# Performance work log

Hardware: AMD Instinct MI355X
Metric: run time of the kernel (lower is better)

Reference implementation:

```python
import jax, jax.numpy as jnp
import numpy as np

EMBED = 256; HEADS = 8; LEVELS = 4; POINTS = 4; DIM = EMBED // HEADS


def _bilinear_gather(vflat, H, W, px, py):
    """grid_sample(mode='bilinear', padding='zeros', align_corners=False).
    vflat: (bs, heads, H*W, d); px, py: (bs, heads, nq, P) pixel coords.
    Returns (bs, heads, nq, P, d).
    """
    x0 = jnp.floor(px); y0 = jnp.floor(py)
    x1 = x0 + 1.0;      y1 = y0 + 1.0
    wx1 = px - x0; wx0 = 1.0 - wx1
    wy1 = py - y0; wy0 = 1.0 - wy1

    def corner(ix, iy, w):
        valid = (ix >= 0) & (ix <= W - 1) & (iy >= 0) & (iy <= H - 1)
        idx = (jnp.clip(iy, 0, H - 1) * W + jnp.clip(ix, 0, W - 1)).astype(jnp.int32)
        b, h, nq, P = idx.shape
        g = jnp.take_along_axis(vflat, idx.reshape(b, h, nq * P)[..., None], axis=2)
        g = g.reshape(b, h, nq, P, -1)
        return g * (w * valid)[..., None]

    return (corner(x0, y0, wx0 * wy0) + corner(x1, y0, wx1 * wy0)
            + corner(x0, y1, wx0 * wy1) + corner(x1, y1, wx1 * wy1))


def _ms_deform_attn(value4, shapes, loc, attn):
    """value4 (bs,nv,heads,D); loc (bs,nq,heads,L,P,2) in [0,1];
    attn (bs,nq,heads,L,P). Returns (bs,nq,heads*D)."""
    bs, nq = loc.shape[0], loc.shape[1]
    grids = 2.0 * loc - 1.0
    attn_t = jnp.transpose(attn, (0, 2, 1, 3, 4))  # (bs,heads,nq,L,P)
    out = jnp.zeros((bs, HEADS, nq, DIM), value4.dtype)
    start = 0
    for lvl in range(LEVELS):
        H, W = int(shapes[lvl, 0]), int(shapes[lvl, 1])
        v = value4[:, start:start + H * W]                 # (bs,HW,heads,D)
        vflat = jnp.transpose(v, (0, 2, 1, 3))             # (bs,heads,HW,D)
        g = jnp.transpose(grids[:, :, :, lvl], (0, 2, 1, 3, 4))  # (bs,heads,nq,P,2)
        px = (g[..., 0] + 1.0) * (W * 0.5) - 0.5
        py = (g[..., 1] + 1.0) * (H * 0.5) - 0.5
        sampled = _bilinear_gather(vflat, H, W, px, py)    # (bs,heads,nq,P,D)
        out = out + jnp.einsum('bhqpd,bhqp->bhqd', sampled, attn_t[:, :, :, lvl])
        start += H * W
    return jnp.transpose(out, (0, 2, 1, 3)).reshape(bs, nq, HEADS * DIM)


def _forward(query, value, query_pos, reference_points, last_reference_offsets,
             shapes, Wv, bv, Wo, bo, Wa, ba, Wout, bout):
    identity = query
    q = query + query_pos
    bs, nq, _ = q.shape
    nv = value.shape[1]
    v = (value @ Wv + bv).reshape(bs, nv, HEADS, DIM)
    off = (q @ Wo + bo).reshape(bs, nq, HEADS, LEVELS, POINTS, 2)
    attn = jax.nn.softmax((q @ Wa + ba).reshape(bs, nq, HEADS, LEVELS * POINTS), axis=-1)
    attn = attn.reshape(bs, nq, HEADS, LEVELS, POINTS)
    wh = jnp.asarray(np.asarray(shapes)[:, ::-1].copy(), jnp.float32)  # (L,2) as (w,h)
    loc = (reference_points[:, :, None, :, None, :]
           + off / wh[None, None, None, :, None, :]
           + last_reference_offsets[:, :, :, None, None, :])  # flow-guided per-head shift
    out = _ms_deform_attn(v, shapes, loc, attn)
    return out @ Wout + bout + identity  # dropout is identity at eval


def setup_inputs() -> dict:
    key = jax.random.key(0)
    ks = jax.random.split(key, 10)
    bs, nq = 8, 1200
    shapes = np.array([[92, 160], [46, 80], [23, 40], [12, 20]], np.int64)
    nv = int((shapes[:, 0] * shapes[:, 1]).sum())
    f = jnp.float32
    return {
        "query": jax.random.normal(ks[0], (bs, nq, EMBED), f),
        "value": jax.random.normal(ks[1], (bs, nv, EMBED), f),
        "query_pos": jax.random.normal(ks[2], (bs, nq, EMBED), f),
        "reference_points": jax.random.uniform(ks[3], (bs, nq, LEVELS, 2), f),
        "last_reference_offsets": jax.random.normal(ks[4], (bs, nq, HEADS, 2), f) * 0.02,
        "spatial_shapes": shapes,
        "Wv": jax.random.normal(ks[5], (EMBED, EMBED), f) * 0.02,
        "bv": jnp.zeros((EMBED,), f),
        "Wo": jax.random.normal(ks[6], (EMBED, HEADS * LEVELS * POINTS * 2), f) * 0.02,
        "bo": jax.random.normal(ks[7], (HEADS * LEVELS * POINTS * 2,), f) * 0.02,
        "Wa": jax.random.normal(ks[8], (EMBED, HEADS * LEVELS * POINTS), f) * 0.02,
        "ba": jnp.zeros((HEADS * LEVELS * POINTS,), f),
        "Wout": jax.random.normal(ks[9], (EMBED, EMBED), f) * 0.02,
        "bout": jnp.zeros((EMBED,), f),
    }


def reference(query, value, query_pos, reference_points, last_reference_offsets,
              spatial_shapes, Wv, bv, Wo, bo, Wa, ba, Wout, bout):
    return _forward(query, value, query_pos, reference_points, last_reference_offsets,
                    spatial_shapes, Wv, bv, Wo, bo, Wa, ba, Wout, bout)
```

## Files before the change

kernel.cpp:

```cpp
#include <hip/hip_runtime.h>
#include <math.h>

#define BS 8
#define NQ 1200
#define NV 19560
#define EMB 256

typedef __bf16 bf16;
typedef bf16 bf16x8 __attribute__((ext_vector_type(8)));
typedef float f32x4 __attribute__((ext_vector_type(4)));
typedef float f32x16 __attribute__((ext_vector_type(16)));

static __device__ __forceinline__ bf16x8 cvt8(float4 a, float4 b) {
    bf16x8 r;
    r[0] = (bf16)a.x; r[1] = (bf16)a.y; r[2] = (bf16)a.z; r[3] = (bf16)a.w;
    r[4] = (bf16)b.x; r[5] = (bf16)b.y; r[6] = (bf16)b.z; r[7] = (bf16)b.w;
    return r;
}

static __device__ __forceinline__ void gl16(const void* g, void* l) {
    __builtin_amdgcn_global_load_lds(
        (const __attribute__((address_space(1))) void*)g,
        (__attribute__((address_space(3))) void*)l, 16, 0, 0);
}

__global__ __launch_bounds__(256) void prep_k(
    const float* __restrict__ Wv, const float* __restrict__ Wo,
    const float* __restrict__ Wa, const float* __restrict__ Wout,
    const float* __restrict__ query, const float* __restrict__ qpos,
    bf16* __restrict__ Wv_p, bf16* __restrict__ Wo_p,
    bf16* __restrict__ Wa_p, bf16* __restrict__ Wout_p, bf16* __restrict__ qsum)
{
    int bid = blockIdx.x, tid = threadIdx.x;
    if (bid < 896) {
        const float* src; bf16* dst; int N, t0;
        if (bid < 256)      { src = Wv;   dst = Wv_p;   N = 256; t0 = bid * 256; }
        else if (bid < 512) { src = Wo;   dst = Wo_p;   N = 256; t0 = (bid - 256) * 256; }
        else if (bid < 640) { src = Wa;   dst = Wa_p;   N = 128; t0 = (bid - 512) * 256; }
        else                { src = Wout; dst = Wout_p; N = 256; t0 = (bid - 640) * 256; }
        int t = t0 + tid;
        int n = t >> 8, k = t & 255;
        dst[t] = (bf16)src[k * N + n];
    } else {
        int t = (bid - 896) * 256 + tid;
        qsum[t] = (bf16)(query[t] + qpos[t]);
    }
}

__global__ __launch_bounds__(256, 1) void vgemm_k(
    const float* __restrict__ A, const bf16* __restrict__ Bp,
    const float* __restrict__ bias, bf16* __restrict__ outB, int Mtiles)
{
    __shared__ __align__(16) bf16 sB[256 * 256];
    const int tid = threadIdx.x;
    const int lane = tid & 63;
    const int w = tid >> 6;
    const int l32 = lane & 31;
    const int hi = lane >> 5;
    const int wr = w >> 1, wc = w & 1;
    const int tstride = gridDim.x;

    float4 buf0[32], buf1[32];
    auto loadA = [&](int t, float4* d) {
        const float* src = A + ((size_t)t * 64 + wr * 32 + l32) * 256 + hi * 8;
#pragma unroll
        for (int ks = 0; ks < 16; ++ks) {
            d[2 * ks]     = *(const float4*)(src + ks * 16);
            d[2 * ks + 1] = *(const float4*)(src + ks * 16 + 4);
        }
    };

    int t0 = blockIdx.x;
    loadA(t0, buf0);

#pragma unroll
    for (int i = 0; i < 32; ++i) {
        int s = i * 256 + tid;
        int r = s >> 5, p = s & 31, c = p ^ (r & 7);
        gl16(Bp + (size_t)r * 256 + c * 8, sB + ((size_t)i * 256 + w * 64) * 8);
    }

    float bb[4];
#pragma unroll
    for (int ct = 0; ct < 4; ++ct) bb[ct] = bias[wc * 128 + ct * 32 + l32];

    __syncthreads();

    auto comp = [&](int t, const float4* d) {
        f32x16 acc[4];
#pragma unroll
        for (int ct = 0; ct < 4; ++ct)
#pragma unroll
            for (int rg = 0; rg < 16; ++rg) acc[ct][rg] = 0.f;
#pragma unroll
        for (int ks = 0; ks < 16; ++ks) {
            bf16x8 af = cvt8(d[2 * ks], d[2 * ks + 1]);
            int p = (ks * 2 + hi) ^ (l32 & 7);
#pragma unroll
            for (int ct = 0; ct < 4; ++ct) {
                int r = wc * 128 + ct * 32 + l32;
                bf16x8 bfr = *(const bf16x8*)(sB + (size_t)r * 256 + p * 8);
                acc[ct] = __builtin_amdgcn_mfma_f32_32x32x16_bf16(af, bfr, acc[ct], 0, 0, 0);
            }
        }
#pragma unroll
        for (int ct = 0; ct < 4; ++ct) {
            int col = wc * 128 + ct * 32 + l32;
#pragma unroll
            for (int rg = 0; rg < 16; ++rg) {
                int row = t * 64 + wr * 32 + (rg & 3) + 8 * (rg >> 2) + 4 * hi;
                outB[(size_t)row * 256 + col] = (bf16)(acc[ct][rg] + bb[ct]);
            }
        }
    };

    int t = t0;
    while (t < Mtiles) {
        int t1 = t + tstride;
        if (t1 < Mtiles) loadA(t1, buf1);
        comp(t, buf0);
        if (t1 >= Mtiles) break;
        int t2 = t1 + tstride;
        if (t2 < Mtiles) loadA(t2, buf0);
        comp(t1, buf1);
        if (t2 >= Mtiles) break;
        t = t2;
    }
}

template <int NS, int NB, bool HAS_RES, bool OUT_BF16>
__global__ __launch_bounds__(256, 2) void gemm3_k(
    const bf16* __restrict__ Ah, const bf16* __restrict__ Bp,
    const float* __restrict__ bias, const float* __restrict__ res,
    float* __restrict__ outF, bf16* __restrict__ outB, int Mtiles)
{
    constexpr int CT = NB / 16;
    __shared__ __align__(16) bf16 sB[NB * 256];
    const int tid = threadIdx.x;
    const int lane = tid & 63;
    const int w = tid >> 6;
    const int l16 = lane & 15;
    const int qd = lane >> 4;
    const int col0 = (blockIdx.x & 1) * NB;
    const int tstride = gridDim.x >> 1;
    const bf16* Bsrc = Bp + (size_t)col0 * 256;

    uint4 curH[8], nxtH[8];
    auto loadA = [&](int t, uint4* dH) {
        size_t rb = ((size_t)t * 64 + w * 16 + l16) * 256;
#pragma unroll
        for (int kc = 0; kc < 8; ++kc)
            dH[kc] = *(const uint4*)(Ah + rb + kc * 32 + qd * 8);
    };

    int tile = blockIdx.x >> 1;
    if (tile < Mtiles) loadA(tile, curH);

#pragma unroll
    for (int i = 0; i < NB * 32 / 256; ++i) {
        int s = i * 256 + tid;
        int r = s >> 5, p = s & 31, c = p ^ (r & 7);
        gl16(Bsrc + (size_t)r * 256 + c * 8, sB + (size_t)(i * 256 + w * 64) * 8);
    }
    __syncthreads();

    for (; tile < Mtiles; tile += tstride) {
        int nt = tile + tstride;
        if (nt < Mtiles) loadA(nt, nxtH);

        f32x4 acc[CT];
#pragma unroll
        for (int c = 0; c < CT; ++c) acc[c] = (f32x4){0.f, 0.f, 0.f, 0.f};
#pragma unroll
        for (int kc = 0; kc < 8; ++kc) {
            bf16x8 af = *(const bf16x8*)&curH[kc];
#pragma unroll
            for (int ct = 0; ct < CT; ++ct) {
                int brow = ct * 16 + l16;
                int chunk = (kc * 4 + qd) ^ (l16 & 7);
                bf16x8 bfr = *(const bf16x8*)(sB + (size_t)brow * 256 + chunk * 8);
                acc[ct] = __builtin_amdgcn_mfma_f32_16x16x32_bf16(af, bfr, acc[ct], 0, 0, 0);
            }
        }
#pragma unroll
        for (int ct = 0; ct < CT; ++ct) {
            int col = col0 + ct * 16 + l16;
            float bbv = bias[col];
#pragma unroll
            for (int r = 0; r < 4; ++r) {
                int row = tile * 64 + w * 16 + qd * 4 + r;
                size_t idx = (size_t)row * NS + col;
                float v = acc[ct][r] + bbv;
                if (HAS_RES) v += res[idx];
                if (OUT_BF16) outB[idx] = (bf16)v;
                else          outF[idx] = v;
            }
        }
#pragma unroll
        for (int i = 0; i < 8; ++i) curH[i] = nxtH[i];
    }
}

static __device__ __forceinline__ void b8f(uint4 u, float* f) {
    f[0] = __uint_as_float(u.x << 16); f[1] = __uint_as_float(u.x & 0xffff0000u);
    f[2] = __uint_as_float(u.y << 16); f[3] = __uint_as_float(u.y & 0xffff0000u);
    f[4] = __uint_as_float(u.z << 16); f[5] = __uint_as_float(u.z & 0xffff0000u);
    f[6] = __uint_as_float(u.w << 16); f[7] = __uint_as_float(u.w & 0xffff0000u);
}

__global__ __launch_bounds__(256) void sample3_k(
    const bf16* __restrict__ vv, const float* __restrict__ offb,
    const float* __restrict__ attnb, const float* __restrict__ refp,
    const float* __restrict__ lref, bf16* __restrict__ outb)
{
    const int cH[4] = {92, 46, 23, 12};
    const int cW[4] = {160, 80, 40, 20};
    const int cS[4] = {0, 14720, 18400, 19320};
    int tid = threadIdx.x;
    int ql = tid >> 5;
    int l32 = tid & 31;
    int h = l32 >> 2, dg = l32 & 3;
    int bq = blockIdx.x * 8 + ql;
    int b = bq / NQ;

    const float* ap = attnb + (size_t)bq * 128 + h * 16;
    float wgt[16];
    float mx = -1e30f;
#pragma unroll
    for (int i = 0; i < 16; i++) { wgt[i] = ap[i]; mx = fmaxf(mx, wgt[i]); }
    float s = 0.f;
#pragma unroll
    for (int i = 0; i < 16; i++) { wgt[i] = __expf(wgt[i] - mx); s += wgt[i]; }
    float inv = 1.f / s;

    const float* rp = refp + (size_t)bq * 8;
    float lrx = lref[(size_t)bq * 16 + h * 2 + 0];
    float lry = lref[(size_t)bq * 16 + h * 2 + 1];
    const float* op = offb + (size_t)bq * 256 + h * 32;

    float acc[8] = {0.f, 0.f, 0.f, 0.f, 0.f, 0.f, 0.f, 0.f};
#pragma unroll
    for (int lvl = 0; lvl < 4; ++lvl) {
        const int Hh = cH[lvl], Ww = cW[lvl];
        const bf16* vb = vv + ((size_t)b * NV + cS[lvl]) * 256 + h * 32 + dg * 8;
        float rx = rp[lvl * 2 + 0], ry = rp[lvl * 2 + 1];
#pragma unroll
        for (int p = 0; p < 4; ++p) {
            float ox = op[lvl * 8 + p * 2 + 0];
            float oy = op[lvl * 8 + p * 2 + 1];
            float px = (rx + ox / (float)Ww + lrx) * (float)Ww - 0.5f;
            float py = (ry + oy / (float)Hh + lry) * (float)Hh - 0.5f;
            float x0f = floorf(px), y0f = floorf(py);
            int x0 = (int)x0f, y0 = (int)y0f;
            float wx1 = px - x0f, wx0 = 1.f - wx1;
            float wy1 = py - y0f, wy0 = 1.f - wy1;
            float ww = wgt[lvl * 4 + p] * inv;
            float w00 = ww * wx0 * wy0, w01 = ww * wx1 * wy0;
            float w10 = ww * wx0 * wy1, w11 = ww * wx1 * wy1;
            bool xa = (unsigned)x0 < (unsigned)Ww;
            bool xb = (unsigned)(x0 + 1) < (unsigned)Ww;
            bool ya = (unsigned)y0 < (unsigned)Hh;
            bool yb = (unsigned)(y0 + 1) < (unsigned)Hh;
            float f[8];
            if (xa && ya) {
                b8f(*(const uint4*)(vb + ((size_t)y0 * Ww + x0) * 256), f);
#pragma unroll
                for (int j = 0; j < 8; j++) acc[j] = fmaf(w00, f[j], acc[j]);
            }
            if (xb && ya) {
                b8f(*(const uint4*)(vb + ((size_t)y0 * Ww + x0 + 1) * 256), f);
#pragma unroll
                for (int j = 0; j < 8; j++) acc[j] = fmaf(w01, f[j], acc[j]);
            }
            if (xa && yb) {
                b8f(*(const uint4*)(vb + ((size_t)(y0 + 1) * Ww + x0) * 256), f);
#pragma unroll
                for (int j = 0; j < 8; j++) acc[j] = fmaf(w10, f[j], acc[j]);
            }
            if (xb && yb) {
                b8f(*(const uint4*)(vb + ((size_t)(y0 + 1) * Ww + x0 + 1) * 256), f);
#pragma unroll
                for (int j = 0; j < 8; j++) acc[j] = fmaf(w11, f[j], acc[j]);
            }
        }
    }
    bf16x8 o;
#pragma unroll
    for (int j = 0; j < 8; j++) o[j] = (bf16)acc[j];
    *(bf16x8*)(outb + (size_t)bq * 256 + h * 32 + dg * 8) = o;
}

extern "C" void kernel_launch(void* const* d_in, const int* in_sizes, int n_in,
                              void* d_out, int out_size, void* d_ws, size_t ws_size,
                              hipStream_t stream) {
    (void)in_sizes; (void)n_in; (void)out_size; (void)ws_size;
    const float* query = (const float*)d_in[0];
    const float* value = (const float*)d_in[1];
    const float* qpos  = (const float*)d_in[2];
    const float* refp  = (const float*)d_in[3];
    const float* lref  = (const float*)d_in[4];
    const float* Wv   = (const float*)d_in[6];
    const float* bv   = (const float*)d_in[7];
    const float* Wo   = (const float*)d_in[8];
    const float* bo   = (const float*)d_in[9];
    const float* Wa   = (const float*)d_in[10];
    const float* ba   = (const float*)d_in[11];
    const float* Wout = (const float*)d_in[12];
    const float* bout = (const float*)d_in[13];

    char* ws = (char*)d_ws;
    bf16*  Wv_p   = (bf16*)(ws + 0);
    bf16*  Wo_p   = (bf16*)(ws + 131072);
    bf16*  Wa_p   = (bf16*)(ws + 262144);
    bf16*  Wout_p = (bf16*)(ws + 327680);
    bf16*  qsum   = (bf16*)(ws + 458752);
    float* off_b  = (float*)(ws + 5373952);
    float* attn_b = (float*)(ws + 15204352);
    bf16*  tsa_b  = (bf16*)(ws + 20119552);
    bf16*  v_b    = (bf16*)(ws + 25034752);

    prep_k<<<10496, 256, 0, stream>>>(Wv, Wo, Wa, Wout, query, qpos,
                                      Wv_p, Wo_p, Wa_p, Wout_p, qsum);

    vgemm_k<<<256, 256, 0, stream>>>(value, Wv_p, bv, v_b, (BS * NV) / 64);
    gemm3_k<256, 128, false, false><<<300, 256, 0, stream>>>(
        qsum, Wo_p, bo, nullptr, off_b, nullptr, (BS * NQ) / 64);
    gemm3_k<128, 64, false, false><<<300, 256, 0, stream>>>(
        qsum, Wa_p, ba, nullptr, attn_b, nullptr, (BS * NQ) / 64);
    sample3_k<<<(BS * NQ) / 8, 256, 0, stream>>>(v_b, off_b, attn_b, refp, lref, tsa_b);
    gemm3_k<256, 128, true, false><<<300, 256, 0, stream>>>(
        tsa_b, Wout_p, bout, query, (float*)d_out, nullptr, (BS * NQ) / 64);
}
```

Before: 416.7 us.

## Parallelize deformable sampling across sampling points with wave-level shuffle reductions

The sampling kernel now gives each 64-lane wave one (query, head) pair, with lanes split over the 16 level/point samples and 4 channel groups, where before one thread looped serially over all 16 samples. Softmax and the final accumulation are done with cross-lane xor shuffles. Corner loads are issued unconditionally at clamped indices, with validity masks folded into the weights, so the four gathers are branch-free and can all be in flight at once. This raises memory-level parallelism and occupancy for the gather-bound kernel. The cost is extra shuffle reductions, 16x more threads, and loads for out-of-bounds corners that were previously skipped.

```diff
diff --git a/kernel.cpp b/kernel.cpp
--- a/kernel.cpp
+++ b/kernel.cpp
@@ -208,7 +208,7 @@
     f[6] = __uint_as_float(u.w << 16); f[7] = __uint_as_float(u.w & 0xffff0000u);
 }
 
-__global__ __launch_bounds__(256) void sample3_k(
+__global__ __launch_bounds__(256) void sample4_k(
     const bf16* __restrict__ vv, const float* __restrict__ offb,
     const float* __restrict__ attnb, const float* __restrict__ refp,
     const float* __restrict__ lref, bf16* __restrict__ outb)
@@ -216,78 +216,78 @@
     const int cH[4] = {92, 46, 23, 12};
     const int cW[4] = {160, 80, 40, 20};
     const int cS[4] = {0, 14720, 18400, 19320};
-    int tid = threadIdx.x;
-    int ql = tid >> 5;
-    int l32 = tid & 31;
-    int h = l32 >> 2, dg = l32 & 3;
-    int bq = blockIdx.x * 8 + ql;
-    int b = bq / NQ;
-
-    const float* ap = attnb + (size_t)bq * 128 + h * 16;
-    float wgt[16];
-    float mx = -1e30f;
-#pragma unroll
-    for (int i = 0; i < 16; i++) { wgt[i] = ap[i]; mx = fmaxf(mx, wgt[i]); }
-    float s = 0.f;
-#pragma unroll
-    for (int i = 0; i < 16; i++) { wgt[i] = __expf(wgt[i] - mx); s += wgt[i]; }
-    float inv = 1.f / s;
-
-    const float* rp = refp + (size_t)bq * 8;
-    float lrx = lref[(size_t)bq * 16 + h * 2 + 0];
+    const int w = threadIdx.x >> 6;
+    const int lane = threadIdx.x & 63;
+    const int wid = blockIdx.x * 4 + w;
+    const int bq = wid >> 3, h = wid & 7;
+    const int b = bq / NQ;
+    const int p = lane >> 2, dg = lane & 3;
+    const int lvl = p >> 2;
+
+    float logit = attnb[(size_t)bq * 128 + h * 16 + p];
+    float mx = logit;
+#pragma unroll
+    for (int s = 4; s < 64; s <<= 1) mx = fmaxf(mx, __shfl_xor(mx, s));
+    float e = __expf(logit - mx);
+    float ssum = e;
+#pragma unroll
+    for (int s = 4; s < 64; s <<= 1) ssum += __shfl_xor(ssum, s);
+    float wgt = e / ssum;
+
+    const int Hh = cH[lvl], Ww = cW[lvl];
+    float ox = offb[(size_t)bq * 256 + h * 32 + p * 2];
+    float oy = offb[(size_t)bq * 256 + h * 32 + p * 2 + 1];
+    float rx = refp[(size_t)bq * 8 + lvl * 2];
+    float ry = refp[(size_t)bq * 8 + lvl * 2 + 1];
+    float lrx = lref[(size_t)bq * 16 + h * 2];
     float lry = lref[(size_t)bq * 16 + h * 2 + 1];
-    const float* op = offb + (size_t)bq * 256 + h * 32;
-
-    float acc[8] = {0.f, 0.f, 0.f, 0.f, 0.f, 0.f, 0.f, 0.f};
-#pragma unroll
-    for (int lvl = 0; lvl < 4; ++lvl) {
-        const int Hh = cH[lvl], Ww = cW[lvl];
-        const bf16* vb = vv + ((size_t)b * NV + cS[lvl]) * 256 + h * 32 + dg * 8;
-        float rx = rp[lvl * 2 + 0], ry = rp[lvl * 2 + 1];
-#pragma unroll
-        for (int p = 0; p < 4; ++p) {
-            float ox = op[lvl * 8 + p * 2 + 0];
-            float oy = op[lvl * 8 + p * 2 + 1];
-            float px = (rx + ox / (float)Ww + lrx) * (float)Ww - 0.5f;
-            float py = (ry + oy / (float)Hh + lry) * (float)Hh - 0.5f;
-            float x0f = floorf(px), y0f = floorf(py);
-            int x0 = (int)x0f, y0 = (int)y0f;
-            float wx1 = px - x0f, wx0 = 1.f - wx1;
-            float wy1 = py - y0f, wy0 = 1.f - wy1;
-            float ww = wgt[lvl * 4 + p] * inv;
-            float w00 = ww * wx0 * wy0, w01 = ww * wx1 * wy0;
-            float w10 = ww * wx0 * wy1, w11 = ww * wx1 * wy1;
-            bool xa = (unsigned)x0 < (unsigned)Ww;
-            bool xb = (unsigned)(x0 + 1) < (unsigned)Ww;
-            bool ya = (unsigned)y0 < (unsigned)Hh;
-            bool yb = (unsigned)(y0 + 1) < (unsigned)Hh;
-            float f[8];
-            if (xa && ya) {
-                b8f(*(const uint4*)(vb + ((size_t)y0 * Ww + x0) * 256), f);
-#pragma unroll
-                for (int j = 0; j < 8; j++) acc[j] = fmaf(w00, f[j], acc[j]);
-            }
-            if (xb && ya) {
-                b8f(*(const uint4*)(vb + ((size_t)y0 * Ww + x0 + 1) * 256), f);
-#pragma unroll
-                for (int j = 0; j < 8; j++) acc[j] = fmaf(w01, f[j], acc[j]);
-            }
-            if (xa && yb) {
-                b8f(*(const uint4*)(vb + ((size_t)(y0 + 1) * Ww + x0) * 256), f);
-#pragma unroll
-                for (int j = 0; j < 8; j++) acc[j] = fmaf(w10, f[j], acc[j]);
-            }
-            if (xb && yb) {
-                b8f(*(const uint4*)(vb + ((size_t)(y0 + 1) * Ww + x0 + 1) * 256), f);
-#pragma unroll
-                for (int j = 0; j < 8; j++) acc[j] = fmaf(w11, f[j], acc[j]);
-            }
-        }
-    }
-    bf16x8 o;
-#pragma unroll
-    for (int j = 0; j < 8; j++) o[j] = (bf16)acc[j];
-    *(bf16x8*)(outb + (size_t)bq * 256 + h * 32 + dg * 8) = o;
+
+    float px = (rx + ox / (float)Ww + lrx) * (float)Ww - 0.5f;
+    float py = (ry + oy / (float)Hh + lry) * (float)Hh - 0.5f;
+    float x0f = floorf(px), y0f = floorf(py);
+    int x0 = (int)x0f, y0 = (int)y0f;
+    float wx1 = px - x0f, wx0 = 1.f - wx1;
+    float wy1 = py - y0f, wy0 = 1.f - wy1;
+    bool xa = (unsigned)x0 < (unsigned)Ww, xb = (unsigned)(x0 + 1) < (unsigned)Ww;
+    bool ya = (unsigned)y0 < (unsigned)Hh, yb = (unsigned)(y0 + 1) < (unsigned)Hh;
+    int xc0 = min(max(x0, 0), Ww - 1), xc1 = min(max(x0 + 1, 0), Ww - 1);
+    int yc0 = min(max(y0, 0), Hh - 1), yc1 = min(max(y0 + 1, 0), Hh - 1);
+    float w00 = wgt * wx0 * wy0 * (float)(xa && ya);
+    float w01 = wgt * wx1 * wy0 * (float)(xb && ya);
+    float w10 = wgt * wx0 * wy1 * (float)(xa && yb);
+    float w11 = wgt * wx1 * wy1 * (float)(xb && yb);
+
+    const bf16* vb = vv + ((size_t)b * NV + cS[lvl]) * 256 + h * 32 + dg * 8;
+    uint4 g00 = *(const uint4*)(vb + ((size_t)yc0 * Ww + xc0) * 256);
+    uint4 g01 = *(const uint4*)(vb + ((size_t)yc0 * Ww + xc1) * 256);
+    uint4 g10 = *(const uint4*)(vb + ((size_t)yc1 * Ww + xc0) * 256);
+    uint4 g11 = *(const uint4*)(vb + ((size_t)yc1 * Ww + xc1) * 256);
+
+    float acc[8], f[8];
+    b8f(g00, f);
+#pragma unroll
+    for (int j = 0; j < 8; j++) acc[j] = w00 * f[j];
+    b8f(g01, f);
+#pragma unroll
+    for (int j = 0; j < 8; j++) acc[j] = fmaf(w01, f[j], acc[j]);
+    b8f(g10, f);
+#pragma unroll
+    for (int j = 0; j < 8; j++) acc[j] = fmaf(w10, f[j], acc[j]);
+    b8f(g11, f);
+#pragma unroll
+    for (int j = 0; j < 8; j++) acc[j] = fmaf(w11, f[j], acc[j]);
+
+#pragma unroll
+    for (int s = 4; s < 64; s <<= 1)
+#pragma unroll
+        for (int j = 0; j < 8; j++) acc[j] += __shfl_xor(acc[j], s);
+
+    if (p == 0) {
+        bf16x8 o;
+#pragma unroll
+        for (int j = 0; j < 8; j++) o[j] = (bf16)acc[j];
+        *(bf16x8*)(outb + (size_t)bq * 256 + h * 32 + dg * 8) = o;
+    }
 }
 
 extern "C" void kernel_launch(void* const* d_in, const int* in_sizes, int n_in,
@@ -327,7 +327,7 @@
         qsum, Wo_p, bo, nullptr, off_b, nullptr, (BS * NQ) / 64);
     gemm3_k<128, 64, false, false><<<300, 256, 0, stream>>>(
         qsum, Wa_p, ba, nullptr, attn_b, nullptr, (BS * NQ) / 64);
-    sample3_k<<<(BS * NQ) / 8, 256, 0, stream>>>(v_b, off_b, attn_b, refp, lref, tsa_b);
+    sample4_k<<<(BS * NQ * 8) / 4, 256, 0, stream>>>(v_b, off_b, attn_b, refp, lref, tsa_b);
     gemm3_k<256, 128, true, false><<<300, 256, 0, stream>>>(
         tsa_b, Wout_p, bout, query, (float*)d_out, nullptr, (BS * NQ) / 64);
 }
```

Result: faster. 399.0 us (-4.2%).
